# Performance work log

Hardware: AMD Instinct MI355X
Metric: run time of the kernel (lower is better)

Reference implementation:

```python
import jax, jax.numpy as jnp
import numpy as np

EPS = 1e-5

def _bn_relu(y, mean, var, scale, bias):
    # y: (b, c, n); eval-mode batchnorm over channel axis, then ReLU
    inv = scale / jnp.sqrt(var + EPS)
    return jax.nn.relu((y - mean[None, :, None]) * inv[None, :, None] + bias[None, :, None])

def setup_inputs() -> dict:
    key = jax.random.key(0)
    ks = jax.random.split(key, 6)
    b, c, n, cr = 4, 256, 4096, 32
    inp = {
        'x': jax.random.normal(ks[0], (b, c, n), jnp.float32),
        'w_q': jax.random.normal(ks[1], (cr, c), jnp.float32) * (1.0 / np.sqrt(c)),
        'w_k': jax.random.normal(ks[2], (cr, c), jnp.float32) * (1.0 / np.sqrt(c)),
        'w_v': jax.random.normal(ks[3], (c, c), jnp.float32) * (1.0 / np.sqrt(c)),
        'bn1_scale': jnp.ones((cr,), jnp.float32), 'bn1_bias': jnp.zeros((cr,), jnp.float32),
        'bn1_mean': jnp.zeros((cr,), jnp.float32), 'bn1_var': jnp.ones((cr,), jnp.float32),
        'bn2_scale': jnp.ones((cr,), jnp.float32), 'bn2_bias': jnp.zeros((cr,), jnp.float32),
        'bn2_mean': jnp.zeros((cr,), jnp.float32), 'bn2_var': jnp.ones((cr,), jnp.float32),
        'bn3_scale': jnp.ones((c,), jnp.float32), 'bn3_bias': jnp.zeros((c,), jnp.float32),
        'bn3_mean': jnp.zeros((c,), jnp.float32), 'bn3_var': jnp.ones((c,), jnp.float32),
        'gamma': jax.random.normal(ks[4], (1,), jnp.float32),
    }
    return inp

def reference(x, w_q, w_k, w_v,
              bn1_scale, bn1_bias, bn1_mean, bn1_var,
              bn2_scale, bn2_bias, bn2_mean, bn2_var,
              bn3_scale, bn3_bias, bn3_mean, bn3_var,
              gamma):
    # x: (b, c, n). Original views as (b, c, n, 1) so width=1, height=n.
    b, c, n = x.shape
    # 1x1 conv == channel matmul, then BN+ReLU
    q = _bn_relu(jnp.einsum('oc,bcn->bon', w_q, x), bn1_mean, bn1_var, bn1_scale, bn1_bias)  # (b, c', n)
    k = _bn_relu(jnp.einsum('oc,bcn->bon', w_k, x), bn2_mean, bn2_var, bn2_scale, bn2_bias)  # (b, c', n)
    v = _bn_relu(jnp.einsum('oc,bcn->bon', w_v, x), bn3_mean, bn3_var, bn3_scale, bn3_bias)  # (b, c, n)
    # energy_H: (b, n, n) with -inf diagonal (self-attention along 'height')
    energy_h = jnp.einsum('bdi,bdj->bij', q, k)
    eye = jnp.eye(n, dtype=bool)
    energy_h = jnp.where(eye[None], -jnp.inf, energy_h)
    # energy_W: width=1 -> per-position self energy (b, n)
    energy_w = jnp.sum(q * k, axis=1)
    # softmax over concat of n H-logits and 1 W-logit
    att = jax.nn.softmax(jnp.concatenate([energy_h, energy_w[..., None]], axis=-1), axis=-1)  # (b, n, n+1)
    att_h = att[..., :n]        # (b, n, n), query i -> key j
    att_w = att[..., n]         # (b, n)
    out_h = jnp.einsum('bcj,bij->bci', v, att_h)   # aggregate values along height
    out_w = v * att_w[:, None, :]                  # width=1 self term
    out = gamma[0] * (out_h + out_w) + x
    return out
```

## Files before the change

### kernel.cpp

```cpp
#include <hip/hip_runtime.h>

#define Bb 4
#define Cc 256
#define Nn 4096
#define CR 32
#define EPS_BN 1e-5f
#define SHIFT2 28.853900817779268f
#define LOG2E  1.4426950408889634f
#define JSPLIT 2
#define JSL (Nn / JSPLIT)
#define TJ 128
#define NTILES (JSL / TJ)

typedef __attribute__((ext_vector_type(8))) short short8;
typedef __attribute__((ext_vector_type(4))) float f32x4;

__device__ inline unsigned int pk2(float a, float b) {
    __bf16 ha = (__bf16)a, hb = (__bf16)b;
    unsigned short ra = __builtin_bit_cast(unsigned short, ha);
    unsigned short rb = __builtin_bit_cast(unsigned short, hb);
    return ((unsigned int)rb << 16) | ra;
}
__device__ inline float blo(unsigned int u) { return __uint_as_float(u << 16); }
__device__ inline float bhi(unsigned int u) { return __uint_as_float(u & 0xffff0000u); }
__device__ inline float ex2(float x) { return __builtin_amdgcn_exp2f(x); }

__global__ __launch_bounds__(256) void prep_kernel(
    const float* __restrict__ x,
    __bf16* __restrict__ xhi, __bf16* __restrict__ xlo,
    const float* __restrict__ wq, const float* __restrict__ wk,
    const float* __restrict__ wv, __bf16* __restrict__ Wf)
{
    __shared__ __align__(16) float tile[64][68];
    const int tid = threadIdx.x;

    if (blockIdx.y == 4) {
        if (blockIdx.z != 0 || blockIdx.x >= 20) return;
        const int r16 = blockIdx.x;
#pragma unroll
        for (int ss = 0; ss < 2; ++ss) {
            int s = tid + ss * 256;
            int kc = s >> 6, lane = s & 63;
            int R = r16 * 16 + (lane & 15);
            const float* src = (R < 32) ? (wq + (size_t)R * Cc)
                             : (R < 64) ? (wk + (size_t)(R - 32) * Cc)
                                        : (wv + (size_t)(R - 64) * Cc);
            const float* p = src + kc * 32 + (lane >> 4) * 8;
            float4 a = *(const float4*)p;
            float4 c2 = *(const float4*)(p + 4);
            uint4 pk = { pk2(a.x,a.y), pk2(a.z,a.w), pk2(c2.x,c2.y), pk2(c2.z,c2.w) };
            *(uint4*)&Wf[(((size_t)r16 * 8 + kc) * 64 + lane) * 8] = pk;
        }
        return;
    }

    const int n0 = blockIdx.x * 64, c0 = blockIdx.y * 64, b = blockIdx.z;

    {
        int r = tid >> 2, q = tid & 3;
        const float* src = &x[(size_t)(b * Cc + c0 + r) * Nn + n0 + q * 16];
#pragma unroll
        for (int u = 0; u < 4; ++u)
            *(float4*)&tile[r][q * 16 + u * 4] = *(const float4*)&src[u * 4];
    }
    __syncthreads();

    {
        int nr = tid >> 2, oc = tid & 3;
        uint4 H[2], L[2];
#pragma unroll
        for (int u = 0; u < 2; ++u) {
            float h[8], lo8[8];
#pragma unroll
            for (int j = 0; j < 8; ++j) {
                float v = tile[oc * 16 + u * 8 + j][nr];
                float hh = (float)(__bf16)v;
                h[j] = hh; lo8[j] = v - hh;
            }
            H[u] = (uint4){ pk2(h[0],h[1]), pk2(h[2],h[3]), pk2(h[4],h[5]), pk2(h[6],h[7]) };
            L[u] = (uint4){ pk2(lo8[0],lo8[1]), pk2(lo8[2],lo8[3]), pk2(lo8[4],lo8[5]), pk2(lo8[6],lo8[7]) };
        }
        size_t base = (size_t)(b * Nn + n0 + nr) * Cc + c0 + oc * 16;
        *(uint4*)&xhi[base]     = H[0];
        *(uint4*)&xhi[base + 8] = H[1];
        *(uint4*)&xlo[base]     = L[0];
        *(uint4*)&xlo[base + 8] = L[1];
    }
}

__global__ __launch_bounds__(256) void qkv_kernel(
    const __bf16* __restrict__ xhi, const __bf16* __restrict__ xlo,
    const __bf16* __restrict__ Wf,
    const float* __restrict__ bn1s, const float* __restrict__ bn1b, const float* __restrict__ bn1m, const float* __restrict__ bn1v,
    const float* __restrict__ bn2s, const float* __restrict__ bn2b, const float* __restrict__ bn2m, const float* __restrict__ bn2v,
    const float* __restrict__ bn3s, const float* __restrict__ bn3b, const float* __restrict__ bn3m, const float* __restrict__ bn3v,
    __bf16* __restrict__ Qt, __bf16* __restrict__ Kt, __bf16* __restrict__ Vb)
{
    __shared__ __align__(16) __bf16 oT[128 * 136];

    const int tid = threadIdx.x;
    const int n0 = blockIdx.x * 128, g = blockIdx.y, b = blockIdx.z;
    const int lane = tid & 63, w = tid >> 6;
    const int l15 = lane & 15, l4 = lane >> 4;
    const int nmt = (g == 0) ? 4 : 8;
    const int r16b = (g == 0) ? 0 : 4 + (g - 1) * 8;

    const size_t bfoff = (size_t)(b * Nn + n0 + w * 32 + l15) * Cc + l4 * 8;
    const __bf16* bh0 = xhi + bfoff;
    const __bf16* bl0 = xlo + bfoff;

    f32x4 acc[8][2];
#pragma unroll
    for (int mt = 0; mt < 8; ++mt)
#pragma unroll
        for (int nt = 0; nt < 2; ++nt) acc[mt][nt] = (f32x4){0.f, 0.f, 0.f, 0.f};

    for (int kc = 0; kc < 8; ++kc) {
        short8 bh[2], bl[2];
#pragma unroll
        for (int nt = 0; nt < 2; ++nt) {
            bh[nt] = *(const short8*)&bh0[(size_t)(nt * 16) * Cc + kc * 32];
            bl[nt] = *(const short8*)&bl0[(size_t)(nt * 16) * Cc + kc * 32];
        }
#pragma unroll
        for (int mt = 0; mt < 8; ++mt) {
            if (mt < nmt) {
                short8 af = *(const short8*)&Wf[(((size_t)(r16b + mt) * 8 + kc) * 64 + lane) * 8];
#pragma unroll
                for (int nt = 0; nt < 2; ++nt) {
                    acc[mt][nt] = __builtin_amdgcn_mfma_f32_16x16x32_bf16(af, bh[nt], acc[mt][nt], 0, 0, 0);
                    acc[mt][nt] = __builtin_amdgcn_mfma_f32_16x16x32_bf16(af, bl[nt], acc[mt][nt], 0, 0, 0);
                }
            }
        }
    }

    if (g == 0) {
#pragma unroll
        for (int mt = 0; mt < 4; ++mt) {
            float scl[4], off[4];
#pragma unroll
            for (int r = 0; r < 4; ++r) {
                int R = mt * 16 + l4 * 4 + r;
                float s, o;
                if (R < 32) {
                    s = bn1s[R] * __frsqrt_rn(bn1v[R] + EPS_BN);
                    o = bn1b[R] - bn1m[R] * s;
                } else {
                    int row = R - 32;
                    s = bn2s[row] * __frsqrt_rn(bn2v[row] + EPS_BN);
                    o = bn2b[row] - bn2m[row] * s;
                    s *= LOG2E; o *= LOG2E;
                }
                scl[r] = s; off[r] = o;
            }
            __bf16* dst = (mt < 2) ? Qt : Kt;
            int d0 = (mt & 1) * 16 + l4 * 4;
#pragma unroll
            for (int nt = 0; nt < 2; ++nt) {
                f32x4 a = acc[mt][nt];
                float e0 = fmaxf(fmaf(a.x, scl[0], off[0]), 0.f);
                float e1 = fmaxf(fmaf(a.y, scl[1], off[1]), 0.f);
                float e2 = fmaxf(fmaf(a.z, scl[2], off[2]), 0.f);
                float e3 = fmaxf(fmaf(a.w, scl[3], off[3]), 0.f);
                uint2 p = { pk2(e0, e1), pk2(e2, e3) };
                int n = n0 + w * 32 + nt * 16 + l15;
                *(uint2*)&dst[(size_t)(b * Nn + n) * CR + d0] = p;
            }
        }
    } else {
        const int vr0 = (g - 1) * 128;
#pragma unroll
        for (int mt = 0; mt < 8; ++mt) {
            float scl[4], off[4];
#pragma unroll
            for (int r = 0; r < 4; ++r) {
                int row = vr0 + mt * 16 + l4 * 4 + r;
                float s = bn3s[row] * __frsqrt_rn(bn3v[row] + EPS_BN);
                scl[r] = s; off[r] = bn3b[row] - bn3m[row] * s;
            }
#pragma unroll
            for (int nt = 0; nt < 2; ++nt) {
                f32x4 a = acc[mt][nt];
                float e[4];
                e[0] = fmaxf(fmaf(a.x, scl[0], off[0]), 0.f);
                e[1] = fmaxf(fmaf(a.y, scl[1], off[1]), 0.f);
                e[2] = fmaxf(fmaf(a.z, scl[2], off[2]), 0.f);
                e[3] = fmaxf(fmaf(a.w, scl[3], off[3]), 0.f);
                int ncol = w * 32 + nt * 16 + l15;
#pragma unroll
                for (int r = 0; r < 4; ++r)
                    oT[(mt * 16 + l4 * 4 + r) * 136 + ncol] = (__bf16)e[r];
            }
        }
        __syncthreads();
        int rr = tid >> 1, qq = tid & 1;
        size_t vrow = (size_t)(b * Cc + vr0 + rr) * Nn + n0 + qq * 64;
#pragma unroll
        for (int e8 = 0; e8 < 8; ++e8)
            *(uint4*)&Vb[vrow + e8 * 8] = *(const uint4*)&oT[rr * 136 + qq * 64 + e8 * 8];
    }
}

__global__ __launch_bounds__(512) void attn_kernel(
    const __bf16* __restrict__ Qt, const __bf16* __restrict__ Kt,
    const __bf16* __restrict__ Vb,
    __bf16* __restrict__ PO, float* __restrict__ PL)
{
    __shared__ __align__(16) __bf16 sQ[64 * 40];
    __shared__ __align__(16) __bf16 sP[64 * 128];
    __shared__ __align__(16) float  sL[8][64];

    const int tid = threadIdx.x, lane = tid & 63, w = tid >> 6;
    const int b = blockIdx.z, js = blockIdx.y, iblk = blockIdx.x;
    const int i0 = iblk * 64;
    const int l15 = lane & 15, l4 = lane >> 4;

    if (tid < 256) {
        int i = tid >> 2, o = tid & 3;
        *(uint4*)&sQ[i * 40 + o * 8] =
            *(const uint4*)&Qt[(size_t)(b * Nn + i0 + i) * CR + o * 8];
    }
    __syncthreads();

    short8 qf[4];
#pragma unroll
    for (int it = 0; it < 4; ++it)
        qf[it] = *(const short8*)&sQ[(it * 16 + l15) * 40 + l4 * 8];

    f32x4 oacc[8];
#pragma unroll
    for (int z = 0; z < 8; ++z) oacc[z] = (f32x4){0.f, 0.f, 0.f, 0.f};
    float lp[4] = {0.f, 0.f, 0.f, 0.f};

    const size_t jb = (size_t)js * JSL;
    short8 kf = *(const short8*)&Kt[(size_t)(b * Nn + jb + 16 * w + l15) * CR + l4 * 8];
    const __bf16* vrow0 = Vb + (size_t)(b * Cc + w * 32 + l15) * Nn;

    char* sPb = (char*)sP;
    const int wcolw = w * 32 + l4 * 8;

    for (int t = 0; t < NTILES; ++t) {
        const size_t j0 = jb + (size_t)t * TJ;

        short8 v0[2], v1[2];
#pragma unroll
        for (int ct = 0; ct < 2; ++ct)
            v0[ct] = *(const short8*)&vrow0[(size_t)(ct * 16) * Nn + j0 + l4 * 8];
#pragma unroll
        for (int ct = 0; ct < 2; ++ct)
            v1[ct] = *(const short8*)&vrow0[(size_t)(ct * 16) * Nn + j0 + 32 + l4 * 8];

#pragma unroll
        for (int it = 0; it < 4; ++it) {
            f32x4 c0 = (f32x4){0.f, 0.f, 0.f, 0.f};
            c0 = __builtin_amdgcn_mfma_f32_16x16x32_bf16(kf, qf[it], c0, 0, 0, 0);
            float e0 = ex2(c0.x - SHIFT2);
            float e1 = ex2(c0.y - SHIFT2);
            float e2 = ex2(c0.z - SHIFT2);
            float e3 = ex2(c0.w - SHIFT2);
            lp[it] += (e0 + e1) + (e2 + e3);
            uint2 p2 = { pk2(e0, e1), pk2(e2, e3) };
            int row = it * 16 + l15;
            *(uint2*)(sPb + row * 256 + (wcolw ^ ((row & 7) << 4))) = p2;
        }
        __syncthreads();

        if (t + 1 < NTILES)
            kf = *(const short8*)&Kt[(size_t)(b * Nn + j0 + TJ + 16 * w + l15) * CR + l4 * 8];

        __builtin_amdgcn_s_setprio(1);
        {
            short8 pf[4];
#pragma unroll
            for (int it = 0; it < 4; ++it) {
                int row = it * 16 + l15;
                pf[it] = *(const short8*)(sPb + row * 256 + ((l4 * 16) ^ ((row & 7) << 4)));
            }
#pragma unroll
            for (int ct = 0; ct < 2; ++ct)
#pragma unroll
                for (int it = 0; it < 4; ++it)
                    oacc[it * 2 + ct] = __builtin_amdgcn_mfma_f32_16x16x32_bf16(
                        pf[it], v0[ct], oacc[it * 2 + ct], 0, 0, 0);
        }
#pragma unroll
        for (int ct = 0; ct < 2; ++ct)
            v0[ct] = *(const short8*)&vrow0[(size_t)(ct * 16) * Nn + j0 + 64 + l4 * 8];
        {
            short8 pf[4];
#pragma unroll
            for (int it = 0; it < 4; ++it) {
                int row = it * 16 + l15;
                pf[it] = *(const short8*)(sPb + row * 256 + ((64 + l4 * 16) ^ ((row & 7) << 4)));
            }
#pragma unroll
            for (int ct = 0; ct < 2; ++ct)
#pragma unroll
                for (int it = 0; it < 4; ++it)
                    oacc[it * 2 + ct] = __builtin_amdgcn_mfma_f32_16x16x32_bf16(
                        pf[it], v1[ct], oacc[it * 2 + ct], 0, 0, 0);
        }
#pragma unroll
        for (int ct = 0; ct < 2; ++ct)
            v1[ct] = *(const short8*)&vrow0[(size_t)(ct * 16) * Nn + j0 + 96 + l4 * 8];
        {
            short8 pf[4];
#pragma unroll
            for (int it = 0; it < 4; ++it) {
                int row = it * 16 + l15;
                pf[it] = *(const short8*)(sPb + row * 256 + ((128 + l4 * 16) ^ ((row & 7) << 4)));
            }
#pragma unroll
            for (int ct = 0; ct < 2; ++ct)
#pragma unroll
                for (int it = 0; it < 4; ++it)
                    oacc[it * 2 + ct] = __builtin_amdgcn_mfma_f32_16x16x32_bf16(
                        pf[it], v0[ct], oacc[it * 2 + ct], 0, 0, 0);
        }
        {
            short8 pf[4];
#pragma unroll
            for (int it = 0; it < 4; ++it) {
                int row = it * 16 + l15;
                pf[it] = *(const short8*)(sPb + row * 256 + ((192 + l4 * 16) ^ ((row & 7) << 4)));
            }
#pragma unroll
            for (int ct = 0; ct < 2; ++ct)
#pragma unroll
                for (int it = 0; it < 4; ++it)
                    oacc[it * 2 + ct] = __builtin_amdgcn_mfma_f32_16x16x32_bf16(
                        pf[it], v1[ct], oacc[it * 2 + ct], 0, 0, 0);
        }
        __builtin_amdgcn_s_setprio(0);
        __syncthreads();
    }

#pragma unroll
    for (int it = 0; it < 4; ++it) {
        float v = lp[it];
        v += __shfl_xor(v, 16);
        v += __shfl_xor(v, 32);
        if (lane < 16) sL[w][it * 16 + lane] = v;
    }
    __syncthreads();
    if (tid < 64) {
        float s = 0.f;
#pragma unroll
        for (int w8 = 0; w8 < 8; ++w8) s += sL[w8][tid];
        PL[(size_t)(js * Bb + b) * Nn + i0 + tid] = s;
    }

    const size_t base = (size_t)((js * Bb + b) * (Nn / 64) + iblk) * 16384;
#pragma unroll
    for (int it = 0; it < 4; ++it)
#pragma unroll
        for (int ct = 0; ct < 2; ++ct) {
            f32x4 a = oacc[it * 2 + ct];
            uint2 p = { pk2(a.x, a.y), pk2(a.z, a.w) };
            int g16 = w * 2 + ct;
            int s = (g16 >> 2) * 16 + it * 4 + (g16 & 3);
            *(uint2*)&PO[base + (size_t)(s * 64 + lane) * 4] = p;
        }
}

__global__ __launch_bounds__(256) void reduce_kernel(
    const __bf16* __restrict__ PO, const float* __restrict__ PL,
    const float* __restrict__ x, const float* __restrict__ gamma,
    float* __restrict__ out)
{
    __shared__ __align__(16) float oT[64 * 68];
    __shared__ float sLinv[64];

    const int tid = threadIdx.x;
    const int iblk = blockIdx.x, wq = blockIdx.y, b = blockIdx.z;
    const int i0 = iblk * 64;
    const int lane = tid & 63, ct = tid >> 6, l15 = lane & 15, l4 = lane >> 4;

    if (tid < 64) {
        float l = 0.f;
#pragma unroll
        for (int js = 0; js < JSPLIT; ++js)
            l += PL[(size_t)(js * Bb + b) * Nn + i0 + tid];
        sLinv[tid] = 1.0f / l;
    }

    float o[4][4];
#pragma unroll
    for (int it = 0; it < 4; ++it) {
        o[it][0] = o[it][1] = o[it][2] = o[it][3] = 0.f;
#pragma unroll
        for (int js = 0; js < JSPLIT; ++js) {
            size_t base = (size_t)((js * Bb + b) * (Nn / 64) + iblk) * 16384;
            uint2 v = *(const uint2*)&PO[base + (size_t)((((wq * 4 + it) * 4 + ct) * 64 + lane)) * 4];
            o[it][0] += blo(v.x); o[it][1] += bhi(v.x);
            o[it][2] += blo(v.y); o[it][3] += bhi(v.y);
        }
    }

    const int cl = ct * 16 + l15;
#pragma unroll
    for (int it = 0; it < 4; ++it) {
        float4 t4 = { o[it][0], o[it][1], o[it][2], o[it][3] };
        *(float4*)&oT[cl * 68 + it * 16 + l4 * 4] = t4;
    }
    __syncthreads();

    const float g = gamma[0];
    const int c_l = tid >> 2, icol = (tid & 3) * 16;
    const int cg = wq * 64 + c_l;
    const size_t gb = (size_t)(b * Cc + cg) * Nn + i0 + icol;
#pragma unroll
    for (int k4 = 0; k4 < 4; ++k4) {
        float4 ov = *(const float4*)&oT[c_l * 68 + icol + k4 * 4];
        float4 li = *(const float4*)&sLinv[icol + k4 * 4];
        float4 xv = *(const float4*)&x[gb + k4 * 4];
        float4 res;
        res.x = fmaf(g, ov.x * li.x, xv.x);
        res.y = fmaf(g, ov.y * li.y, xv.y);
        res.z = fmaf(g, ov.z * li.z, xv.z);
        res.w = fmaf(g, ov.w * li.w, xv.w);
        *(float4*)&out[gb + k4 * 4] = res;
    }
}

extern "C" void kernel_launch(void* const* d_in, const int* in_sizes, int n_in,
                              void* d_out, int out_size, void* d_ws, size_t ws_size,
                              hipStream_t stream)
{
    const float* x    = (const float*)d_in[0];
    const float* wq   = (const float*)d_in[1];
    const float* wk   = (const float*)d_in[2];
    const float* wv   = (const float*)d_in[3];
    const float* bn1s = (const float*)d_in[4];
    const float* bn1b = (const float*)d_in[5];
    const float* bn1m = (const float*)d_in[6];
    const float* bn1v = (const float*)d_in[7];
    const float* bn2s = (const float*)d_in[8];
    const float* bn2b = (const float*)d_in[9];
    const float* bn2m = (const float*)d_in[10];
    const float* bn2v = (const float*)d_in[11];
    const float* bn3s = (const float*)d_in[12];
    const float* bn3b = (const float*)d_in[13];
    const float* bn3m = (const float*)d_in[14];
    const float* bn3v = (const float*)d_in[15];
    const float* gmm  = (const float*)d_in[16];
    float* out = (float*)d_out;

    char* ws = (char*)d_ws;
    __bf16* Qt  = (__bf16*)(ws);
    __bf16* Kt  = (__bf16*)(ws + (1u << 20));
    __bf16* Vb  = (__bf16*)(ws + (2u << 20));
    __bf16* PO  = (__bf16*)(ws + (10u << 20));
    float*  PL  = (float*)(ws + (26u << 20));
    __bf16* Wf  = (__bf16*)(ws + (26u << 20) + 262144);
    __bf16* xhi = (__bf16*)(ws + (27u << 20));
    __bf16* xlo = (__bf16*)(ws + (35u << 20));

    prep_kernel<<<dim3(Nn / 64, 5, Bb), 256, 0, stream>>>(
        x, xhi, xlo, wq, wk, wv, Wf);

    qkv_kernel<<<dim3(Nn / 128, 3, Bb), 256, 0, stream>>>(
        xhi, xlo, Wf,
        bn1s, bn1b, bn1m, bn1v,
        bn2s, bn2b, bn2m, bn2v,
        bn3s, bn3b, bn3m, bn3v,
        Qt, Kt, Vb);

    attn_kernel<<<dim3(Nn / 64, JSPLIT, Bb), 512, 0, stream>>>(Qt, Kt, Vb, PO, PL);

    reduce_kernel<<<dim3(Nn / 64, 4, Bb), 256, 0, stream>>>(PO, PL, x, gmm, out);
}
```

Baseline: 202.0 us.

## Keep attention probabilities in registers via ds_bpermute instead of LDS staging

Rewrites the attention kernel so each wave owns 16 query rows and half the value channels. Probabilities are rearranged from the QK MFMA output layout into the PV MFMA input layout with ds_bpermute, removing the shared-memory P tile and the per-tile block barriers. The cost is that QK and exp work is recomputed once per channel half, and the grid now covers 128 queries per block with a channel split. Each wave also streams more V rows per step, which raises register pressure.

```diff
diff --git a/kernel.cpp b/kernel.cpp
--- a/kernel.cpp
+++ b/kernel.cpp
@@ -9,11 +9,11 @@
 #define LOG2E  1.4426950408889634f
 #define JSPLIT 2
 #define JSL (Nn / JSPLIT)
-#define TJ 128
-#define NTILES (JSL / TJ)
+#define JT32 (JSL / 32)
 
 typedef __attribute__((ext_vector_type(8))) short short8;
 typedef __attribute__((ext_vector_type(4))) float f32x4;
+typedef __attribute__((ext_vector_type(4))) int int4v;
 
 __device__ inline unsigned int pk2(float a, float b) {
     __bf16 ha = (__bf16)a, hb = (__bf16)b;
@@ -207,161 +207,88 @@
     const __bf16* __restrict__ Vb,
     __bf16* __restrict__ PO, float* __restrict__ PL)
 {
-    __shared__ __align__(16) __bf16 sQ[64 * 40];
-    __shared__ __align__(16) __bf16 sP[64 * 128];
-    __shared__ __align__(16) float  sL[8][64];
-
     const int tid = threadIdx.x, lane = tid & 63, w = tid >> 6;
-    const int b = blockIdx.z, js = blockIdx.y, iblk = blockIdx.x;
-    const int i0 = iblk * 64;
+    const int b = blockIdx.z, iblk = blockIdx.x;
+    const int js = blockIdx.y >> 1, cs = blockIdx.y & 1;
     const int l15 = lane & 15, l4 = lane >> 4;
 
-    if (tid < 256) {
-        int i = tid >> 2, o = tid & 3;
-        *(uint4*)&sQ[i * 40 + o * 8] =
-            *(const uint4*)&Qt[(size_t)(b * Nn + i0 + i) * CR + o * 8];
-    }
-    __syncthreads();
-
-    short8 qf[4];
-#pragma unroll
-    for (int it = 0; it < 4; ++it)
-        qf[it] = *(const short8*)&sQ[(it * 16 + l15) * 40 + l4 * 8];
+    const int i0 = iblk * 128 + w * 16;
+    const short8 qf = *(const short8*)&Qt[(size_t)(b * Nn + i0 + l15) * CR + l4 * 8];
 
     f32x4 oacc[8];
 #pragma unroll
     for (int z = 0; z < 8; ++z) oacc[z] = (f32x4){0.f, 0.f, 0.f, 0.f};
-    float lp[4] = {0.f, 0.f, 0.f, 0.f};
+    float lp = 0.f;
 
     const size_t jb = (size_t)js * JSL;
-    short8 kf = *(const short8*)&Kt[(size_t)(b * Nn + jb + 16 * w + l15) * CR + l4 * 8];
-    const __bf16* vrow0 = Vb + (size_t)(b * Cc + w * 32 + l15) * Nn;
-
-    char* sPb = (char*)sP;
-    const int wcolw = w * 32 + l4 * 8;
-
-    for (int t = 0; t < NTILES; ++t) {
-        const size_t j0 = jb + (size_t)t * TJ;
-
-        short8 v0[2], v1[2];
-#pragma unroll
-        for (int ct = 0; ct < 2; ++ct)
-            v0[ct] = *(const short8*)&vrow0[(size_t)(ct * 16) * Nn + j0 + l4 * 8];
-#pragma unroll
-        for (int ct = 0; ct < 2; ++ct)
-            v1[ct] = *(const short8*)&vrow0[(size_t)(ct * 16) * Nn + j0 + 32 + l4 * 8];
-
-#pragma unroll
-        for (int it = 0; it < 4; ++it) {
-            f32x4 c0 = (f32x4){0.f, 0.f, 0.f, 0.f};
-            c0 = __builtin_amdgcn_mfma_f32_16x16x32_bf16(kf, qf[it], c0, 0, 0, 0);
-            float e0 = ex2(c0.x - SHIFT2);
-            float e1 = ex2(c0.y - SHIFT2);
-            float e2 = ex2(c0.z - SHIFT2);
-            float e3 = ex2(c0.w - SHIFT2);
-            lp[it] += (e0 + e1) + (e2 + e3);
-            uint2 p2 = { pk2(e0, e1), pk2(e2, e3) };
-            int row = it * 16 + l15;
-            *(uint2*)(sPb + row * 256 + (wcolw ^ ((row & 7) << 4))) = p2;
-        }
-        __syncthreads();
-
-        if (t + 1 < NTILES)
-            kf = *(const short8*)&Kt[(size_t)(b * Nn + j0 + TJ + 16 * w + l15) * CR + l4 * 8];
-
-        __builtin_amdgcn_s_setprio(1);
-        {
-            short8 pf[4];
-#pragma unroll
-            for (int it = 0; it < 4; ++it) {
-                int row = it * 16 + l15;
-                pf[it] = *(const short8*)(sPb + row * 256 + ((l4 * 16) ^ ((row & 7) << 4)));
-            }
-#pragma unroll
-            for (int ct = 0; ct < 2; ++ct)
-#pragma unroll
-                for (int it = 0; it < 4; ++it)
-                    oacc[it * 2 + ct] = __builtin_amdgcn_mfma_f32_16x16x32_bf16(
-                        pf[it], v0[ct], oacc[it * 2 + ct], 0, 0, 0);
-        }
-#pragma unroll
-        for (int ct = 0; ct < 2; ++ct)
-            v0[ct] = *(const short8*)&vrow0[(size_t)(ct * 16) * Nn + j0 + 64 + l4 * 8];
-        {
-            short8 pf[4];
-#pragma unroll
-            for (int it = 0; it < 4; ++it) {
-                int row = it * 16 + l15;
-                pf[it] = *(const short8*)(sPb + row * 256 + ((64 + l4 * 16) ^ ((row & 7) << 4)));
-            }
-#pragma unroll
-            for (int ct = 0; ct < 2; ++ct)
-#pragma unroll
-                for (int it = 0; it < 4; ++it)
-                    oacc[it * 2 + ct] = __builtin_amdgcn_mfma_f32_16x16x32_bf16(
-                        pf[it], v1[ct], oacc[it * 2 + ct], 0, 0, 0);
-        }
-#pragma unroll
-        for (int ct = 0; ct < 2; ++ct)
-            v1[ct] = *(const short8*)&vrow0[(size_t)(ct * 16) * Nn + j0 + 96 + l4 * 8];
-        {
-            short8 pf[4];
-#pragma unroll
-            for (int it = 0; it < 4; ++it) {
-                int row = it * 16 + l15;
-                pf[it] = *(const short8*)(sPb + row * 256 + ((128 + l4 * 16) ^ ((row & 7) << 4)));
-            }
-#pragma unroll
-            for (int ct = 0; ct < 2; ++ct)
-#pragma unroll
-                for (int it = 0; it < 4; ++it)
-                    oacc[it * 2 + ct] = __builtin_amdgcn_mfma_f32_16x16x32_bf16(
-                        pf[it], v0[ct], oacc[it * 2 + ct], 0, 0, 0);
-        }
-        {
-            short8 pf[4];
-#pragma unroll
-            for (int it = 0; it < 4; ++it) {
-                int row = it * 16 + l15;
-                pf[it] = *(const short8*)(sPb + row * 256 + ((192 + l4 * 16) ^ ((row & 7) << 4)));
-            }
-#pragma unroll
-            for (int ct = 0; ct < 2; ++ct)
-#pragma unroll
-                for (int it = 0; it < 4; ++it)
-                    oacc[it * 2 + ct] = __builtin_amdgcn_mfma_f32_16x16x32_bf16(
-                        pf[it], v1[ct], oacc[it * 2 + ct], 0, 0, 0);
-        }
-        __builtin_amdgcn_s_setprio(0);
-        __syncthreads();
-    }
-
-#pragma unroll
-    for (int it = 0; it < 4; ++it) {
-        float v = lp[it];
-        v += __shfl_xor(v, 16);
-        v += __shfl_xor(v, 32);
-        if (lane < 16) sL[w][it * 16 + lane] = v;
-    }
-    __syncthreads();
-    if (tid < 64) {
-        float s = 0.f;
-#pragma unroll
-        for (int w8 = 0; w8 < 8; ++w8) s += sL[w8][tid];
-        PL[(size_t)(js * Bb + b) * Nn + i0 + tid] = s;
-    }
-
-    const size_t base = (size_t)((js * Bb + b) * (Nn / 64) + iblk) * 16384;
-#pragma unroll
-    for (int it = 0; it < 4; ++it)
-#pragma unroll
-        for (int ct = 0; ct < 2; ++ct) {
-            f32x4 a = oacc[it * 2 + ct];
-            uint2 p = { pk2(a.x, a.y), pk2(a.z, a.w) };
-            int g16 = w * 2 + ct;
-            int s = (g16 >> 2) * 16 + it * 4 + (g16 & 3);
-            *(uint2*)&PO[base + (size_t)(s * 64 + lane) * 4] = p;
-        }
+    const __bf16* krow  = Kt + (size_t)(b * Nn + jb + l15) * CR + l4 * 8;
+    const __bf16* vrow0 = Vb + (size_t)(b * Cc + cs * 128 + l15) * Nn + jb + l4 * 8;
+
+    const int s0 = (l15 + ((l4 & 1) << 5)) << 2;
+    const int s1 = s0 + 64;
+    const bool hiq = (lane >= 32);
+
+    short8 kf0 = *(const short8*)&krow[0];
+    short8 kf1 = *(const short8*)&krow[16 * CR];
+
+    for (int jt = 0; jt < JT32; ++jt) {
+        const int joff = jt * 32;
+
+        short8 vf[8];
+#pragma unroll
+        for (int ct = 0; ct < 8; ++ct)
+            vf[ct] = *(const short8*)&vrow0[(size_t)(ct * 16) * Nn + joff];
+
+        short8 kn0 = kf0, kn1 = kf1;
+        if (jt + 1 < JT32) {
+            kn0 = *(const short8*)&krow[(joff + 32) * CR];
+            kn1 = *(const short8*)&krow[(joff + 48) * CR];
+        }
+
+        f32x4 c0 = (f32x4){0.f, 0.f, 0.f, 0.f};
+        f32x4 c1 = (f32x4){0.f, 0.f, 0.f, 0.f};
+        c0 = __builtin_amdgcn_mfma_f32_16x16x32_bf16(kf0, qf, c0, 0, 0, 0);
+        c1 = __builtin_amdgcn_mfma_f32_16x16x32_bf16(kf1, qf, c1, 0, 0, 0);
+        float e0 = ex2(c0.x - SHIFT2), e1 = ex2(c0.y - SHIFT2);
+        float e2 = ex2(c0.z - SHIFT2), e3 = ex2(c0.w - SHIFT2);
+        float f0 = ex2(c1.x - SHIFT2), f1 = ex2(c1.y - SHIFT2);
+        float f2 = ex2(c1.z - SHIFT2), f3 = ex2(c1.w - SHIFT2);
+        lp += ((e0 + e1) + (e2 + e3)) + ((f0 + f1) + (f2 + f3));
+        int q0u0 = (int)pk2(e0, e1), q0u1 = (int)pk2(e2, e3);
+        int q1u0 = (int)pk2(f0, f1), q1u1 = (int)pk2(f2, f3);
+
+        int A0 = __builtin_amdgcn_ds_bpermute(s0, q0u0);
+        int A1 = __builtin_amdgcn_ds_bpermute(s0, q0u1);
+        int A2 = __builtin_amdgcn_ds_bpermute(s1, q0u0);
+        int A3 = __builtin_amdgcn_ds_bpermute(s1, q0u1);
+        int B0 = __builtin_amdgcn_ds_bpermute(s0, q1u0);
+        int B1 = __builtin_amdgcn_ds_bpermute(s0, q1u1);
+        int B2 = __builtin_amdgcn_ds_bpermute(s1, q1u0);
+        int B3 = __builtin_amdgcn_ds_bpermute(s1, q1u1);
+        int4v ww = { hiq ? B0 : A0, hiq ? B1 : A1, hiq ? B2 : A2, hiq ? B3 : A3 };
+        short8 paf = __builtin_bit_cast(short8, ww);
+
+#pragma unroll
+        for (int ct = 0; ct < 8; ++ct)
+            oacc[ct] = __builtin_amdgcn_mfma_f32_16x16x32_bf16(paf, vf[ct], oacc[ct], 0, 0, 0);
+
+        kf0 = kn0; kf1 = kn1;
+    }
+
+    lp += __shfl_xor(lp, 16);
+    lp += __shfl_xor(lp, 32);
+    if (cs == 0 && lane < 16)
+        PL[(size_t)(js * Bb + b) * Nn + i0 + lane] = lp;
+
+    const size_t pbase = (size_t)((js * Bb + b) * (Nn / 64) + 2 * iblk + (w >> 2)) * 16384;
+#pragma unroll
+    for (int ct = 0; ct < 8; ++ct) {
+        f32x4 a = oacc[ct];
+        uint2 p = { pk2(a.x, a.y), pk2(a.z, a.w) };
+        int gc = cs * 8 + ct;
+        int s = ((gc >> 2) * 4 + (w & 3)) * 4 + (gc & 3);
+        *(uint2*)&PO[pbase + (size_t)(s * 64 + lane) * 4] = p;
+    }
 }
 
 __global__ __launch_bounds__(256) void reduce_kernel(
@@ -467,7 +394,7 @@
         bn3s, bn3b, bn3m, bn3v,
         Qt, Kt, Vb);
 
-    attn_kernel<<<dim3(Nn / 64, JSPLIT, Bb), 512, 0, stream>>>(Qt, Kt, Vb, PO, PL);
+    attn_kernel<<<dim3(Nn / 128, JSPLIT * 2, Bb), 512, 0, stream>>>(Qt, Kt, Vb, PO, PL);
 
     reduce_kernel<<<dim3(Nn / 64, 4, Bb), 256, 0, stream>>>(PO, PL, x, gmm, out);
 }
```

Measured after the change: 391.0 us. 1.94x slower.
